# Kernel optimization log

Hardware: AMD Instinct MI355X
Metric: run time of the kernel (lower is better)

Reference implementation:

```python
import math
import jax, jax.numpy as jnp
import numpy as np

B, C, H, W = 16, 512, 32, 32
NUM_HEADS = 4
GROUPS = 32
EPS = 1e-5


def setup_inputs() -> dict:
    key = jax.random.key(0)
    ks = jax.random.split(key, 3)
    x = jax.random.normal(ks[0], (B, C, H, W), dtype=jnp.float32)
    # conv weights: kaiming-ish scale for 1x1 convs (fan_in = C)
    qkv_w = jax.random.normal(ks[1], (3 * C, C), dtype=jnp.float32) * (1.0 / math.sqrt(C))
    proj_w = jax.random.normal(ks[2], (C, C), dtype=jnp.float32) * (1.0 / math.sqrt(C))
    return {
        "x": x,
        "norm_w": jnp.ones((C,), jnp.float32),
        "norm_b": jnp.zeros((C,), jnp.float32),
        "qkv_w": qkv_w,
        "qkv_b": jnp.zeros((3 * C,), jnp.float32),
        "proj_w": proj_w,
        "proj_b": jnp.zeros((C,), jnp.float32),
    }


def group_norm(x, w, b):
    bN, c, h, wd = x.shape
    xg = x.reshape(bN, GROUPS, c // GROUPS, h, wd)
    mean = xg.mean(axis=(2, 3, 4), keepdims=True)
    var = xg.var(axis=(2, 3, 4), keepdims=True)
    xg = (xg - mean) * jax.lax.rsqrt(var + EPS)
    x = xg.reshape(bN, c, h, wd)
    return x * w[None, :, None, None] + b[None, :, None, None]


def conv1x1(x, w, b):
    # x: (b,c,h,w), w: (out,in), b: (out,)
    return jnp.einsum('bchw,oc->bohw', x, w) + b[None, :, None, None]


def reference(x, norm_w, norm_b, qkv_w, qkv_b, proj_w, proj_b):
    b, c, h, w = x.shape
    hd = c // NUM_HEADS  # head dim
    n = h * w            # tokens
    qkv = conv1x1(group_norm(x, norm_w, norm_b), qkv_w, qkv_b)
    q, k, v = jnp.split(qkv, 3, axis=1)
    # (b, heads, hd, n)
    q = q.reshape(b, NUM_HEADS, hd, n)
    k = k.reshape(b, NUM_HEADS, hd, n)
    v = v.reshape(b, NUM_HEADS, hd, n)
    # attn: (b, heads, n, n)
    attn = jnp.einsum('bhdn,bhdm->bhnm', q, k) / math.sqrt(hd)
    attn = jax.nn.softmax(attn, axis=-1)
    # out: (b, heads, n, hd) -> (b, c, h, w)
    out = jnp.einsum('bhnm,bhdm->bhnd', attn, v)
    out = out.transpose(0, 1, 3, 2).reshape(b, c, h, w)
    return x + conv1x1(out, proj_w, proj_b)
```

## Files before the change

### kernel.cpp

```cpp
#include <hip/hip_runtime.h>
#include <stdint.h>

#define DEV __device__ __forceinline__

typedef __attribute__((ext_vector_type(4))) float f32x4;
typedef __attribute__((ext_vector_type(8))) short s16x8;
typedef __attribute__((ext_vector_type(8))) __bf16 bf16x8;

constexpr int kB = 16, kC = 512, kN = 1024;
constexpr int kO = 1536;
constexpr int kG = 32, kCPG = 16;
constexpr float kEps = 1e-5f;
constexpr float kQS = 0.08838834764831845f * 1.44269504088896f;

#if __has_builtin(__builtin_amdgcn_exp2f)
#define EXP2(x) __builtin_amdgcn_exp2f(x)
#else
#define EXP2(x) exp2f(x)
#endif

DEV unsigned short f2bf(float f) {
  union { float f; uint32_t u; } cv; cv.f = f;
  uint32_t u = cv.u;
  return (unsigned short)((u + 0x7FFFu + ((u >> 16) & 1u)) >> 16);
}

DEV unsigned short bfbits(float f) {
  __bf16 h = (__bf16)f;
  return __builtin_bit_cast(unsigned short, h);
}

DEV bf16x8 asbf(s16x8 v) { return __builtin_bit_cast(bf16x8, v); }

DEV void gl_lds16(const void* g, void* l) {
  __builtin_amdgcn_global_load_lds(
      (const __attribute__((address_space(1))) uint32_t*)g,
      (__attribute__((address_space(3))) uint32_t*)l, 16, 0, 0);
}

__global__ __launch_bounds__(256) void k_wconv2(const float* __restrict__ qw,
                                                const float* __restrict__ pw,
                                                unsigned short* __restrict__ dq,
                                                unsigned short* __restrict__ dp) {
  const int nq = 1536 * 512 / 4, np = 512 * 512 / 4;
  int i = blockIdx.x * 256 + threadIdx.x;
  const float* src;
  unsigned short* dst;
  int j;
  if (i < nq) { src = qw; dst = dq; j = i; }
  else { j = i - nq; if (j >= np) return; src = pw; dst = dp; }
  f32x4 v = ((const f32x4*)src)[j];
  unsigned short o[4];
  o[0] = f2bf(v[0]); o[1] = f2bf(v[1]); o[2] = f2bf(v[2]); o[3] = f2bf(v[3]);
  ((uint2*)dst)[j] = *(uint2*)o;
}

__global__ __launch_bounds__(256) void k_gnstats(const float* __restrict__ x,
                                                 float* __restrict__ meanp,
                                                 float* __restrict__ rstdp) {
  int bg = blockIdx.x;
  const f32x4* p4 = (const f32x4*)(x + (size_t)bg * (kCPG * kN));
  float s = 0.f, s2 = 0.f;
  for (int i = threadIdx.x; i < (kCPG * kN / 4); i += 256) {
    f32x4 v = p4[i];
    s += v[0] + v[1] + v[2] + v[3];
    s2 += v[0] * v[0] + v[1] * v[1] + v[2] * v[2] + v[3] * v[3];
  }
#pragma unroll
  for (int m = 32; m >= 1; m >>= 1) { s += __shfl_xor(s, m); s2 += __shfl_xor(s2, m); }
  __shared__ float rb[8];
  int lane = threadIdx.x & 63, wid = threadIdx.x >> 6;
  if (lane == 0) { rb[wid * 2] = s; rb[wid * 2 + 1] = s2; }
  __syncthreads();
  if (threadIdx.x == 0) {
    float S = rb[0] + rb[2] + rb[4] + rb[6];
    float S2 = rb[1] + rb[3] + rb[5] + rb[7];
    float mu = S * (1.f / 16384.f);
    float var = S2 * (1.f / 16384.f) - mu * mu;
    meanp[bg] = mu;
    rstdp[bg] = rsqrtf(var + kEps);
  }
}

__global__ __launch_bounds__(256) void k_gnapply(const float* __restrict__ x,
                                                 const float* __restrict__ gw,
                                                 const float* __restrict__ gb,
                                                 const float* __restrict__ meanp,
                                                 const float* __restrict__ rstdp,
                                                 unsigned short* __restrict__ xt) {
  int bid = blockIdx.x;
  int b = bid >> 7;
  int ct = (bid >> 4) & 7;
  int nt = bid & 15;
  int c0 = ct * 64, n0 = nt * 64;
  __shared__ float tile[64][65];
  int t = threadIdx.x;
#pragma unroll
  for (int pass = 0; pass < 4; ++pass) {
    int r = pass * 16 + (t >> 4);
    int col = (t & 15) << 2;
    int c = c0 + r;
    f32x4 v = *(const f32x4*)(x + ((size_t)b * kC + c) * kN + n0 + col);
    int g = b * kG + (c >> 4);
    float rs = rstdp[g];
    float a = rs * gw[c];
    float bb = gb[c] - meanp[g] * a;
    tile[r][col + 0] = v[0] * a + bb;
    tile[r][col + 1] = v[1] * a + bb;
    tile[r][col + 2] = v[2] * a + bb;
    tile[r][col + 3] = v[3] * a + bb;
  }
  __syncthreads();
#pragma unroll
  for (int pass = 0; pass < 2; ++pass) {
    int nr = pass * 32 + (t >> 3);
    int cb = (t & 7) << 3;
    unsigned short o[8];
#pragma unroll
    for (int j = 0; j < 8; ++j) o[j] = f2bf(tile[cb + j][nr]);
    *(uint4*)(xt + ((size_t)b * kN + n0 + nr) * kC + c0 + cb) = *(uint4*)o;
  }
}

template <int MODE>
__global__ __launch_bounds__(256, 3) void k_gemm(const unsigned short* __restrict__ act,
                                                 const unsigned short* __restrict__ wb,
                                                 const float* __restrict__ bias,
                                                 unsigned short* __restrict__ qkT,
                                                 unsigned short* __restrict__ vbuf,
                                                 const float* __restrict__ xres,
                                                 float* __restrict__ outp) {
  int b = blockIdx.y;
  int nt = blockIdx.x & 7, ot = blockIdx.x >> 3;
  int n0 = nt << 7, o0 = ot << 7;
  int t = threadIdx.x, lane = t & 63, wid = t >> 6;
  int wr = wid >> 1, wc = wid & 1;
  __shared__ __align__(16) char smem[49152];
  f32x4 acc[4][4];
  const f32x4 zf = {0.f, 0.f, 0.f, 0.f};
#pragma unroll
  for (int i = 0; i < 4; ++i)
#pragma unroll
    for (int j = 0; j < 4; ++j) acc[i][j] = zf;
  const size_t rowb = (size_t)b * kN;

  auto stage = [&](int buf, int kt2) {
    const int k0 = kt2 << 5;
    char* dA = smem + buf * 8192;
    char* dB = smem + 24576 + buf * 8192;
#pragma unroll
    for (int p = 0; p < 2; ++p) {
      const int id = p * 256 + t;
      const int row = id >> 2, cp = id & 3;
      const int cl = cp ^ ((row >> 1) & 3);
      gl_lds16(act + (rowb + n0 + row) * (size_t)kC + k0 + cl * 8, dA + id * 16);
      gl_lds16(wb + (size_t)(o0 + row) * kC + k0 + cl * 8, dB + id * 16);
    }
  };

  stage(0, 0);
  stage(1, 1);
  int cur = 0, stg = 2;
#pragma unroll 1
  for (int kt = 0; kt < 16; ++kt) {
    if (kt < 15) {
      asm volatile("s_waitcnt vmcnt(4)" ::: "memory");
    } else {
      asm volatile("s_waitcnt vmcnt(0)" ::: "memory");
    }
    __builtin_amdgcn_s_barrier();
    if (kt < 14) stage(stg, kt + 2);
    const char* pA = smem + cur * 8192;
    const char* pB = smem + 24576 + cur * 8192;
    s16x8 af[4], bfr[4];
    const int c = lane >> 4;
#pragma unroll
    for (int i = 0; i < 4; ++i) {
      const int rA = wr * 64 + i * 16 + (lane & 15);
      af[i] = *(const s16x8*)(pA + rA * 64 + ((c ^ ((rA >> 1) & 3)) << 4));
      const int rB = wc * 64 + i * 16 + (lane & 15);
      bfr[i] = *(const s16x8*)(pB + rB * 64 + ((c ^ ((rB >> 1) & 3)) << 4));
    }
    __builtin_amdgcn_s_setprio(1);
#pragma unroll
    for (int i = 0; i < 4; ++i)
#pragma unroll
      for (int j = 0; j < 4; ++j)
        acc[i][j] = __builtin_amdgcn_mfma_f32_16x16x32_bf16(asbf(af[i]), asbf(bfr[j]),
                                                            acc[i][j], 0, 0, 0);
    __builtin_amdgcn_s_setprio(0);
    cur = (cur == 2) ? 0 : cur + 1;
    stg = (stg == 2) ? 0 : stg + 1;
  }

  if (MODE == 0) {
    if (o0 < 1024) {
      __syncthreads();
      const float sc = (o0 < 512) ? kQS : 1.0f;
      unsigned short* tile = (unsigned short*)smem;
#pragma unroll
      for (int j = 0; j < 4; ++j) {
        const int o = wc * 64 + j * 16 + (lane & 15);
        const float bs = bias[o0 + o];
#pragma unroll
        for (int i = 0; i < 4; ++i)
#pragma unroll
          for (int r = 0; r < 4; ++r) {
            const int n = wr * 64 + i * 16 + ((lane >> 4) << 2) + r;
            tile[n * 136 + o] = f2bf((acc[i][j][r] + bs) * sc);
          }
      }
      __syncthreads();
#pragma unroll
      for (int it = 0; it < 8; ++it) {
        const int n = it * 16 + (t >> 4);
        const int c8 = t & 15;
        *(uint4*)(qkT + (rowb + n0 + n) * (size_t)kO + o0 + c8 * 8) =
            *(const uint4*)(tile + n * 136 + c8 * 8);
      }
    } else {
#pragma unroll
      for (int j = 0; j < 4; ++j) {
        const int o = o0 + wc * 64 + j * 16 + (lane & 15);
        const float bs = bias[o];
#pragma unroll
        for (int i = 0; i < 4; ++i) {
          const int nb = n0 + wr * 64 + ((lane >> 4) << 2) + i * 16;
          unsigned short pk[4];
#pragma unroll
          for (int r = 0; r < 4; ++r) pk[r] = f2bf(acc[i][j][r] + bs);
          *(uint2*)(vbuf + ((size_t)b * 512 + (o - 1024)) * kN + nb) = *(uint2*)pk;
        }
      }
    }
  } else {
    const int baseN = n0 + wr * 64 + ((lane >> 4) << 2);
#pragma unroll
    for (int j = 0; j < 4; ++j) {
      const int o = o0 + wc * 64 + j * 16 + (lane & 15);
      const float bs = bias[o];
#pragma unroll
      for (int i = 0; i < 4; ++i) {
        const int nb = baseN + i * 16;
        const size_t oo = ((size_t)b * kC + o) * kN + nb;
        const f32x4 xv = *(const f32x4*)(xres + oo);
        f32x4 ov;
        ov[0] = acc[i][j][0] + bs + xv[0];
        ov[1] = acc[i][j][1] + bs + xv[1];
        ov[2] = acc[i][j][2] + bs + xv[2];
        ov[3] = acc[i][j][3] + bs + xv[3];
        *(f32x4*)(outp + oo) = ov;
      }
    }
  }
}

__global__ __launch_bounds__(256, 2) void k_attn(const unsigned short* __restrict__ qkT,
                                                 const unsigned short* __restrict__ vbuf,
                                                 unsigned short* __restrict__ aoT) {
  const int bh = blockIdx.x, qt = blockIdx.y;
  const int b = bh >> 2, h = bh & 3;
  const int t = threadIdx.x, lane = t & 63, wid = t >> 6;
  __shared__ unsigned short sK[2][64 * 128];
  __shared__ unsigned short sV[2][128 * 64];
  __shared__ unsigned short sP[128 * 64];
  const int qrow0 = qt * 128 + wid * 32;
  s16x8 qf[2][4];
#pragma unroll
  for (int bi = 0; bi < 2; ++bi)
#pragma unroll
    for (int kk = 0; kk < 4; ++kk)
      qf[bi][kk] = *(const s16x8*)(qkT + ((size_t)b * kN + qrow0 + bi * 16 + (lane & 15)) * kO +
                                   h * 128 + kk * 32 + ((lane >> 4) << 3));
  f32x4 oc[2][8];
  const f32x4 zf = {0.f, 0.f, 0.f, 0.f};
#pragma unroll
  for (int bi = 0; bi < 2; ++bi)
#pragma unroll
    for (int dj = 0; dj < 8; ++dj) oc[bi][dj] = zf;
  float lpart[8];
#pragma unroll
  for (int i = 0; i < 8; ++i) lpart[i] = 0.f;

  auto stage = [&](int buf, int m0) {
#pragma unroll
    for (int p = 0; p < 4; ++p) {
      const int id = p * 256 + t;
      {
        const int row = id >> 4, cp = id & 15, cl = cp ^ (row & 7);
        gl_lds16(qkT + ((size_t)b * kN + m0 + row) * kO + 512 + h * 128 + cl * 8,
                 (char*)sK[buf] + (p * 256 + wid * 64) * 16);
      }
      {
        const int row = id >> 3, cp = id & 7, cl = cp ^ (row & 7);
        gl_lds16(vbuf + ((size_t)b * 512 + h * 128 + row) * kN + m0 + cl * 8,
                 (char*)sV[buf] + (p * 256 + wid * 64) * 16);
      }
    }
  };

  stage(0, 0);
#pragma unroll 1
  for (int mt = 0; mt < 16; ++mt) {
    const int cur = mt & 1;
    asm volatile("s_waitcnt vmcnt(0)" ::: "memory");
    __syncthreads();
    if (mt < 15) stage(cur ^ 1, (mt + 1) * 64);
    f32x4 sacc[2][4];
#pragma unroll
    for (int bi = 0; bi < 2; ++bi)
#pragma unroll
      for (int j = 0; j < 4; ++j) sacc[bi][j] = zf;
    __builtin_amdgcn_s_setprio(1);
#pragma unroll
    for (int kk = 0; kk < 4; ++kk) {
      s16x8 kf[4];
      const int cl = kk * 4 + (lane >> 4);
#pragma unroll
      for (int j = 0; j < 4; ++j) {
        const int rm = j * 16 + (lane & 15);
        kf[j] = *(const s16x8*)((const char*)sK[cur] + rm * 256 + ((cl ^ (rm & 7)) << 4));
      }
#pragma unroll
      for (int bi = 0; bi < 2; ++bi)
#pragma unroll
        for (int j = 0; j < 4; ++j)
          sacc[bi][j] = __builtin_amdgcn_mfma_f32_16x16x32_bf16(asbf(qf[bi][kk]), asbf(kf[j]),
                                                                sacc[bi][j], 0, 0, 0);
    }
    __builtin_amdgcn_s_setprio(0);
#pragma unroll
    for (int bi = 0; bi < 2; ++bi)
#pragma unroll
      for (int r = 0; r < 4; ++r) {
        const int nrow = wid * 32 + bi * 16 + ((lane >> 4) << 2) + r;
        float pvs = 0.f;
#pragma unroll
        for (int j = 0; j < 4; ++j) {
          const float p = EXP2(sacc[bi][j][r]);
          pvs += p;
          const int m = j * 16 + (lane & 15);
          *(unsigned short*)((char*)sP + nrow * 128 + (((m >> 3) ^ (nrow & 7)) << 4) +
                             ((m & 7) << 1)) = bfbits(p);
        }
        lpart[bi * 4 + r] += pvs;
      }
    __builtin_amdgcn_s_setprio(1);
#pragma unroll
    for (int ks = 0; ks < 2; ++ks) {
      s16x8 pf[2], vf[8];
      const int cl = ks * 4 + (lane >> 4);
#pragma unroll
      for (int bi = 0; bi < 2; ++bi) {
        const int rp = wid * 32 + bi * 16 + (lane & 15);
        pf[bi] = *(const s16x8*)((const char*)sP + rp * 128 + ((cl ^ (rp & 7)) << 4));
      }
#pragma unroll
      for (int dj = 0; dj < 8; ++dj) {
        const int rv = dj * 16 + (lane & 15);
        vf[dj] = *(const s16x8*)((const char*)sV[cur] + rv * 128 + ((cl ^ (rv & 7)) << 4));
      }
#pragma unroll
      for (int bi = 0; bi < 2; ++bi)
#pragma unroll
        for (int dj = 0; dj < 8; ++dj)
          oc[bi][dj] = __builtin_amdgcn_mfma_f32_16x16x32_bf16(asbf(pf[bi]), asbf(vf[dj]),
                                                               oc[bi][dj], 0, 0, 0);
    }
    __builtin_amdgcn_s_setprio(0);
  }
#pragma unroll
  for (int bi = 0; bi < 2; ++bi) {
#pragma unroll
    for (int r = 0; r < 4; ++r) {
      float ls = lpart[bi * 4 + r];
#pragma unroll
      for (int st = 1; st <= 8; st <<= 1) ls += __shfl_xor(ls, st);
      const float inv = 1.f / ls;
      const int n = qrow0 + bi * 16 + ((lane >> 4) << 2) + r;
#pragma unroll
      for (int dj = 0; dj < 8; ++dj) {
        const int d = dj * 16 + (lane & 15);
        aoT[((size_t)b * kN + n) * kC + h * 128 + d] = bfbits(oc[bi][dj][r] * inv);
      }
    }
  }
}

extern "C" void kernel_launch(void* const* d_in, const int* in_sizes, int n_in,
                              void* d_out, int out_size, void* d_ws, size_t ws_size,
                              hipStream_t stream) {
  const float* x = (const float*)d_in[0];
  const float* norm_w = (const float*)d_in[1];
  const float* norm_b = (const float*)d_in[2];
  const float* qkv_w = (const float*)d_in[3];
  const float* qkv_b = (const float*)d_in[4];
  const float* proj_w = (const float*)d_in[5];
  const float* proj_b = (const float*)d_in[6];
  float* out = (float*)d_out;
  char* ws = (char*)d_ws;
  const size_t OFF_MEAN = 0;
  const size_t OFF_RSTD = 2048;
  const size_t OFF_WQ = 4096;
  const size_t OFF_WP = OFF_WQ + (size_t)1536 * 512 * 2;
  const size_t OFF_XT = OFF_WP + (size_t)512 * 512 * 2;
  const size_t OFF_QKT = OFF_XT + (size_t)16 * 1024 * 512 * 2;
  const size_t OFF_V = OFF_QKT + (size_t)16 * 1024 * 1536 * 2;
  const size_t NEED = OFF_V + (size_t)16 * 512 * 1024 * 2;
  if (ws_size < NEED) return;
  float* meanp = (float*)(ws + OFF_MEAN);
  float* rstdp = (float*)(ws + OFF_RSTD);
  unsigned short* wq = (unsigned short*)(ws + OFF_WQ);
  unsigned short* wp = (unsigned short*)(ws + OFF_WP);
  unsigned short* xt = (unsigned short*)(ws + OFF_XT);
  unsigned short* qkT = (unsigned short*)(ws + OFF_QKT);
  unsigned short* vb = (unsigned short*)(ws + OFF_V);
  unsigned short* aoT = xt;

  k_wconv2<<<1024, 256, 0, stream>>>(qkv_w, proj_w, wq, wp);
  k_gnstats<<<512, 256, 0, stream>>>(x, meanp, rstdp);
  k_gnapply<<<2048, 256, 0, stream>>>(x, norm_w, norm_b, meanp, rstdp, xt);
  k_gemm<0><<<dim3(96, 16), 256, 0, stream>>>(xt, wq, qkv_b, qkT, vb, nullptr, nullptr);
  k_attn<<<dim3(64, 8), 256, 0, stream>>>(qkT, vb, aoT);
  k_gemm<1><<<dim3(32, 16), 256, 0, stream>>>(aoT, wp, proj_b, nullptr, nullptr, x, out);
}
```

Baseline: 125.3 us.

## Switch attention to 32x32x16 MFMA and keep P in registers via permlane swap

Rewrites the attention kernel's QK^T and PV stages to use 32x32x16 bf16 MFMA tiles. It computes S transposed (K as A operand) so the exp'd probabilities can be packed with v_cvt_pk_bf16_f32 and rearranged with v_permlane32_swap into the A-operand layout for PV. This removes the round trip of P through shared memory and reduces LDS traffic and the number of MFMA issues. The row-sum normalization now goes through a small shared buffer, and that read happens without a barrier after the write.

```diff
diff --git a/kernel.cpp b/kernel.cpp
--- a/kernel.cpp
+++ b/kernel.cpp
@@ -4,6 +4,7 @@
 #define DEV __device__ __forceinline__
 
 typedef __attribute__((ext_vector_type(4))) float f32x4;
+typedef __attribute__((ext_vector_type(16))) float f32x16;
 typedef __attribute__((ext_vector_type(8))) short s16x8;
 typedef __attribute__((ext_vector_type(8))) __bf16 bf16x8;
 
@@ -31,6 +32,12 @@
 }
 
 DEV bf16x8 asbf(s16x8 v) { return __builtin_bit_cast(bf16x8, v); }
+
+DEV uint32_t cvtpk(float a, float b) {
+  uint32_t w;
+  asm("v_cvt_pk_bf16_f32 %0, %1, %2" : "=v"(w) : "v"(a), "v"(b));
+  return w;
+}
 
 DEV void gl_lds16(const void* g, void* l) {
   __builtin_amdgcn_global_load_lds(
@@ -261,26 +268,22 @@
   const int bh = blockIdx.x, qt = blockIdx.y;
   const int b = bh >> 2, h = bh & 3;
   const int t = threadIdx.x, lane = t & 63, wid = t >> 6;
+  const int l31 = lane & 31, hi = lane >> 5;
   __shared__ unsigned short sK[2][64 * 128];
   __shared__ unsigned short sV[2][128 * 64];
-  __shared__ unsigned short sP[128 * 64];
+  __shared__ float sL[4][32];
   const int qrow0 = qt * 128 + wid * 32;
-  s16x8 qf[2][4];
-#pragma unroll
-  for (int bi = 0; bi < 2; ++bi)
-#pragma unroll
-    for (int kk = 0; kk < 4; ++kk)
-      qf[bi][kk] = *(const s16x8*)(qkT + ((size_t)b * kN + qrow0 + bi * 16 + (lane & 15)) * kO +
-                                   h * 128 + kk * 32 + ((lane >> 4) << 3));
-  f32x4 oc[2][8];
-  const f32x4 zf = {0.f, 0.f, 0.f, 0.f};
-#pragma unroll
-  for (int bi = 0; bi < 2; ++bi)
-#pragma unroll
-    for (int dj = 0; dj < 8; ++dj) oc[bi][dj] = zf;
-  float lpart[8];
-#pragma unroll
-  for (int i = 0; i < 8; ++i) lpart[i] = 0.f;
+  s16x8 qf[8];
+#pragma unroll
+  for (int kk = 0; kk < 8; ++kk)
+    qf[kk] = *(const s16x8*)(qkT + ((size_t)b * kN + qrow0 + l31) * kO + h * 128 +
+                             kk * 16 + hi * 8);
+  f32x16 oc[4];
+#pragma unroll
+  for (int df = 0; df < 4; ++df)
+#pragma unroll
+    for (int r = 0; r < 16; ++r) oc[df][r] = 0.f;
+  float lpart = 0.f;
 
   auto stage = [&](int buf, int m0) {
 #pragma unroll
@@ -306,83 +309,80 @@
     asm volatile("s_waitcnt vmcnt(0)" ::: "memory");
     __syncthreads();
     if (mt < 15) stage(cur ^ 1, (mt + 1) * 64);
-    f32x4 sacc[2][4];
-#pragma unroll
-    for (int bi = 0; bi < 2; ++bi)
-#pragma unroll
-      for (int j = 0; j < 4; ++j) sacc[bi][j] = zf;
+    f32x16 sa0, sa1;
+#pragma unroll
+    for (int r = 0; r < 16; ++r) { sa0[r] = 0.f; sa1[r] = 0.f; }
     __builtin_amdgcn_s_setprio(1);
 #pragma unroll
-    for (int kk = 0; kk < 4; ++kk) {
-      s16x8 kf[4];
-      const int cl = kk * 4 + (lane >> 4);
-#pragma unroll
-      for (int j = 0; j < 4; ++j) {
-        const int rm = j * 16 + (lane & 15);
-        kf[j] = *(const s16x8*)((const char*)sK[cur] + rm * 256 + ((cl ^ (rm & 7)) << 4));
-      }
-#pragma unroll
-      for (int bi = 0; bi < 2; ++bi)
-#pragma unroll
-        for (int j = 0; j < 4; ++j)
-          sacc[bi][j] = __builtin_amdgcn_mfma_f32_16x16x32_bf16(asbf(qf[bi][kk]), asbf(kf[j]),
-                                                                sacc[bi][j], 0, 0, 0);
+    for (int kk = 0; kk < 8; ++kk) {
+      const int c0 = kk * 2 + hi;
+      const int r0 = l31, r1 = 32 + l31;
+      s16x8 kf0 = *(const s16x8*)((const char*)sK[cur] + r0 * 256 + ((c0 ^ (r0 & 7)) << 4));
+      s16x8 kf1 = *(const s16x8*)((const char*)sK[cur] + r1 * 256 + ((c0 ^ (r1 & 7)) << 4));
+      sa0 = __builtin_amdgcn_mfma_f32_32x32x16_bf16(asbf(kf0), asbf(qf[kk]), sa0, 0, 0, 0);
+      sa1 = __builtin_amdgcn_mfma_f32_32x32x16_bf16(asbf(kf1), asbf(qf[kk]), sa1, 0, 0, 0);
     }
     __builtin_amdgcn_s_setprio(0);
-#pragma unroll
-    for (int bi = 0; bi < 2; ++bi)
-#pragma unroll
-      for (int r = 0; r < 4; ++r) {
-        const int nrow = wid * 32 + bi * 16 + ((lane >> 4) << 2) + r;
-        float pvs = 0.f;
-#pragma unroll
-        for (int j = 0; j < 4; ++j) {
-          const float p = EXP2(sacc[bi][j][r]);
-          pvs += p;
-          const int m = j * 16 + (lane & 15);
-          *(unsigned short*)((char*)sP + nrow * 128 + (((m >> 3) ^ (nrow & 7)) << 4) +
-                             ((m & 7) << 1)) = bfbits(p);
-        }
-        lpart[bi * 4 + r] += pvs;
-      }
+    float p0[16], p1[16];
+    float ps = 0.f;
+#pragma unroll
+    for (int r = 0; r < 16; ++r) { p0[r] = EXP2(sa0[r]); ps += p0[r]; }
+#pragma unroll
+    for (int r = 0; r < 16; ++r) { p1[r] = EXP2(sa1[r]); ps += p1[r]; }
+    lpart += ps;
+    uint32_t paw[4][4];
+#pragma unroll
+    for (int half = 0; half < 2; ++half) {
+      const int base = half * 8;
+      {
+        uint32_t a0 = cvtpk(p0[base + 0], p0[base + 1]);
+        uint32_t b0 = cvtpk(p0[base + 4], p0[base + 5]);
+        asm volatile("v_permlane32_swap_b32 %0, %1" : "+v"(a0), "+v"(b0));
+        uint32_t a1 = cvtpk(p0[base + 2], p0[base + 3]);
+        uint32_t b1 = cvtpk(p0[base + 6], p0[base + 7]);
+        asm volatile("v_permlane32_swap_b32 %0, %1" : "+v"(a1), "+v"(b1));
+        paw[half][0] = a0; paw[half][1] = a1; paw[half][2] = b0; paw[half][3] = b1;
+      }
+      {
+        uint32_t a0 = cvtpk(p1[base + 0], p1[base + 1]);
+        uint32_t b0 = cvtpk(p1[base + 4], p1[base + 5]);
+        asm volatile("v_permlane32_swap_b32 %0, %1" : "+v"(a0), "+v"(b0));
+        uint32_t a1 = cvtpk(p1[base + 2], p1[base + 3]);
+        uint32_t b1 = cvtpk(p1[base + 6], p1[base + 7]);
+        asm volatile("v_permlane32_swap_b32 %0, %1" : "+v"(a1), "+v"(b1));
+        paw[2 + half][0] = a0; paw[2 + half][1] = a1; paw[2 + half][2] = b0; paw[2 + half][3] = b1;
+      }
+    }
     __builtin_amdgcn_s_setprio(1);
 #pragma unroll
-    for (int ks = 0; ks < 2; ++ks) {
-      s16x8 pf[2], vf[8];
-      const int cl = ks * 4 + (lane >> 4);
-#pragma unroll
-      for (int bi = 0; bi < 2; ++bi) {
-        const int rp = wid * 32 + bi * 16 + (lane & 15);
-        pf[bi] = *(const s16x8*)((const char*)sP + rp * 128 + ((cl ^ (rp & 7)) << 4));
-      }
-#pragma unroll
-      for (int dj = 0; dj < 8; ++dj) {
-        const int rv = dj * 16 + (lane & 15);
-        vf[dj] = *(const s16x8*)((const char*)sV[cur] + rv * 128 + ((cl ^ (rv & 7)) << 4));
-      }
-#pragma unroll
-      for (int bi = 0; bi < 2; ++bi)
-#pragma unroll
-        for (int dj = 0; dj < 8; ++dj)
-          oc[bi][dj] = __builtin_amdgcn_mfma_f32_16x16x32_bf16(asbf(pf[bi]), asbf(vf[dj]),
-                                                               oc[bi][dj], 0, 0, 0);
+    for (int ks = 0; ks < 4; ++ks) {
+      union { uint32_t w[4]; s16x8 v; } pa;
+      pa.w[0] = paw[ks][0]; pa.w[1] = paw[ks][1]; pa.w[2] = paw[ks][2]; pa.w[3] = paw[ks][3];
+      const int cv = ks * 2 + hi;
+#pragma unroll
+      for (int df = 0; df < 4; ++df) {
+        const int rv = df * 32 + l31;
+        s16x8 vf = *(const s16x8*)((const char*)sV[cur] + rv * 128 + ((cv ^ (rv & 7)) << 4));
+        oc[df] = __builtin_amdgcn_mfma_f32_32x32x16_bf16(asbf(pa.v), asbf(vf), oc[df], 0, 0, 0);
+      }
     }
     __builtin_amdgcn_s_setprio(0);
   }
-#pragma unroll
-  for (int bi = 0; bi < 2; ++bi) {
-#pragma unroll
-    for (int r = 0; r < 4; ++r) {
-      float ls = lpart[bi * 4 + r];
-#pragma unroll
-      for (int st = 1; st <= 8; st <<= 1) ls += __shfl_xor(ls, st);
-      const float inv = 1.f / ls;
-      const int n = qrow0 + bi * 16 + ((lane >> 4) << 2) + r;
-#pragma unroll
-      for (int dj = 0; dj < 8; ++dj) {
-        const int d = dj * 16 + (lane & 15);
-        aoT[((size_t)b * kN + n) * kC + h * 128 + d] = bfbits(oc[bi][dj][r] * inv);
-      }
+  lpart += __shfl_xor(lpart, 32);
+  if (hi == 0) sL[wid][l31] = lpart;
+  float inv[16];
+#pragma unroll
+  for (int r = 0; r < 16; ++r) {
+    const int crow = (r & 3) + 8 * (r >> 2) + 4 * hi;
+    inv[r] = 1.f / sL[wid][crow];
+  }
+#pragma unroll
+  for (int df = 0; df < 4; ++df) {
+    const int d = df * 32 + l31;
+#pragma unroll
+    for (int r = 0; r < 16; ++r) {
+      const int n = qrow0 + (r & 3) + 8 * (r >> 2) + 4 * hi;
+      aoT[((size_t)b * kN + n) * kC + h * 128 + d] = bfbits(oc[df][r] * inv[r]);
     }
   }
 }
```

New measurement: 121.0 us. 3.4% less time.
